# Optimization experiments

Hardware: AMD Instinct MI355X
Metric: run time of the kernel (lower is better)

The kernel has to match this reference:

```python
import jax, jax.numpy as jnp
import numpy as np

N = 131072   # total nodes in batch
D = 128      # hidden dim (in_dim = out_dim = 128)
DX = 64      # raw node feature dim (x and rw_feature each)
NG = 1024    # number of graphs (global_add_pool segments)
E = 4194304  # edges per hop adjacency (avg degree 32)
H = 4        # num_hops + 1 MLP branches per layer


def setup_inputs() -> dict:
    key = jax.random.key(0)
    ks = jax.random.split(key, 16)
    s = 0.05
    return {
        "x": jax.random.normal(ks[0], (N, DX), jnp.float32),
        "rw_feature": jax.random.normal(ks[1], (N, DX), jnp.float32),
        "hop1_features": jax.random.normal(ks[2], (N, D), jnp.float32),
        "hop2_features": jax.random.normal(ks[3], (N, D), jnp.float32),
        "hop3_features": jax.random.normal(ks[4], (N, D), jnp.float32),
        "hop1_edges": jax.random.randint(ks[5], (2, E), 0, N, dtype=jnp.int32),
        "hop2_edges": jax.random.randint(ks[6], (2, E), 0, N, dtype=jnp.int32),
        "hop3_edges": jax.random.randint(ks[7], (2, E), 0, N, dtype=jnp.int32),
        "batch": jnp.sort(jax.random.randint(ks[8], (N,), 0, NG, dtype=jnp.int32)),
        "l1_w1": jax.random.normal(ks[9], (H, D, D), jnp.float32) * s,
        "l1_b1": jnp.zeros((H, D), jnp.float32),
        "l1_w2": jax.random.normal(ks[10], (H, D, D), jnp.float32) * s,
        "l1_b2": jnp.zeros((H, D), jnp.float32),
        "l2_w1": jax.random.normal(ks[11], (H, D, D), jnp.float32) * s,
        "l2_b1": jnp.zeros((H, D), jnp.float32),
        "l2_w2": jax.random.normal(ks[12], (H, D, D), jnp.float32) * s,
        "l2_b2": jnp.zeros((H, D), jnp.float32),
        "lin_w": jax.random.normal(ks[13], (2 * D, D), jnp.float32) * s,
        "lin_b": jnp.zeros((D,), jnp.float32),
    }


def _mhc_layer(hops, w1, b1, w2, b2):
    # hops: [H, N, D]; per-hop MLP (Linear -> ReLU -> Dropout(eval) -> Linear), summed over hops
    z = jax.nn.relu(jnp.einsum('hni,hio->hno', hops, w1) + b1[:, None, :])
    y = jnp.einsum('hno,hop->hnp', z, w2) + b2[:, None, :]
    return jnp.sum(y, axis=0)  # [N, D]


def _spmm(edges, x):
    # torch.sparse.mm(A, x) with A[r, c] = 1.0 per edge; duplicate edges accumulate (COO sum)
    return jax.ops.segment_sum(x[edges[1]], edges[0], num_segments=N)


def reference(x, rw_feature, hop1_features, hop2_features, hop3_features,
              hop1_edges, hop2_edges, hop3_edges, batch,
              l1_w1, l1_b1, l1_w2, l1_b2, l2_w1, l2_b1, l2_w2, l2_b2,
              lin_w, lin_b):
    f = jnp.concatenate([x, rw_feature], axis=1)  # [N, D]
    h1 = jnp.stack([f, hop1_features, hop2_features, hop3_features], axis=0)  # [H, N, D]
    x1 = _mhc_layer(h1, l1_w1, l1_b1, l1_w2, l1_b2)
    h2 = jnp.stack([x1,
                    _spmm(hop1_edges, x1),
                    _spmm(hop2_edges, x1),
                    _spmm(hop3_edges, x1)], axis=0)
    x2 = _mhc_layer(h2, l2_w1, l2_b1, l2_w2, l2_b2)
    out = jnp.concatenate([x1, x2], axis=1) @ lin_w + lin_b  # concat=True path
    return jax.ops.segment_sum(out, batch, num_segments=NG)  # global_add_pool -> [NG, D]
```

## Files before the change

### kernel.cpp

```cpp
#include <hip/hip_runtime.h>

#define N_NODES 131072
#define DIM     128
#define NGRAPH  1024
#define NEDGE   4194304

#define NW      512
#define WBINS   256
#define NSL     256
#define SLICE_E (NEDGE / NSL)
#define CAP     12288

typedef float floatx4 __attribute__((ext_vector_type(4)));
typedef float f32x4  __attribute__((ext_vector_type(4)));
typedef __bf16 bf16x8 __attribute__((ext_vector_type(8)));
typedef __bf16 bf16x4 __attribute__((ext_vector_type(4)));

__device__ __forceinline__ int lds_off(int row, int kb) {
    return row * 256 + (kb ^ ((row & 7) << 4));
}

#define GLOAD16(gp, lp) __builtin_amdgcn_global_load_lds( \
    (const __attribute__((address_space(1))) void*)(gp),  \
    (__attribute__((address_space(3))) void*)(lp), 16, 0, 0)

__device__ __forceinline__ void stage_async(char* dstbase, const char* src,
                                            int w, int lane) {
#pragma unroll
    for (int it = 0; it < 8; ++it) {
        int chunk = it * 4 + w;
        int p = chunk * 1024 + lane * 16;
        int r = p >> 8;
        int o = p & 255;
        const char* g = src + r * 256 + (o ^ ((r & 7) << 4));
        GLOAD16(g, dstbase + chunk * 1024);
    }
}

__global__ __launch_bounds__(256)
void zero_kernel(floatx4* __restrict__ p, long n4) {
    long i = (long)blockIdx.x * blockDim.x + threadIdx.x;
    long stride = (long)gridDim.x * blockDim.x;
    floatx4 z = {0.f, 0.f, 0.f, 0.f};
    for (; i < n4; i += stride) p[i] = z;
}

__global__ __launch_bounds__(256)
void cvt_kernel(const float* __restrict__ src, __bf16* __restrict__ dst) {
    int i = blockIdx.x * 256 + threadIdx.x;
    const int stride = gridDim.x * 256;
    const int total = N_NODES * 32;
    for (; i < total; i += stride) {
        floatx4 v = ((const floatx4*)src)[i];
        bf16x4 h;
        h[0] = (__bf16)v[0]; h[1] = (__bf16)v[1];
        h[2] = (__bf16)v[2]; h[3] = (__bf16)v[3];
        ((bf16x4*)dst)[i] = h;
    }
}

__global__ __launch_bounds__(256)
void cvt_cat_kernel(const float* __restrict__ x, const float* __restrict__ rw,
                    __bf16* __restrict__ dst) {
    int i = blockIdx.x * 256 + threadIdx.x;
    const int stride = gridDim.x * 256;
    const int total = N_NODES * 32;
    for (; i < total; i += stride) {
        int rowg = i >> 5, g = i & 31;
        const float* s = (g < 16) ? x  + (size_t)rowg * 64 + g * 4
                                  : rw + (size_t)rowg * 64 + (g - 16) * 4;
        floatx4 v = *(const floatx4*)s;
        bf16x4 h;
        h[0] = (__bf16)v[0]; h[1] = (__bf16)v[1];
        h[2] = (__bf16)v[2]; h[3] = (__bf16)v[3];
        *(bf16x4*)(dst + (size_t)rowg * 128 + g * 4) = h;
    }
}

__global__ __launch_bounds__(256)
void tr_kernel(const float* __restrict__ src, __bf16* __restrict__ dst, int nmat) {
    int idx = blockIdx.x * blockDim.x + threadIdx.x;
    int total = nmat * 16384;
    if (idx >= total) return;
    int m = idx >> 14;
    int col = (idx >> 7) & 127;
    int k = idx & 127;
    dst[idx] = (__bf16)src[m * 16384 + k * 128 + col];
}

__global__ __launch_bounds__(256)
void wincount_kernel(const int* __restrict__ e1, const int* __restrict__ e2,
                     const int* __restrict__ e3, int* __restrict__ gcount) {
    const int gb = blockIdx.x;
    const int sl = gb % NSL;
    const int hop = gb / NSL;
    const int* rows = hop == 0 ? e1 : hop == 1 ? e2 : e3;

    __shared__ int cnt[NW];
    for (int i = threadIdx.x; i < NW; i += 256) cnt[i] = 0;
    __syncthreads();

    const int4* src = (const int4*)rows + (size_t)sl * (SLICE_E / 4);
    for (int j = threadIdx.x; j < SLICE_E / 4; j += 256) {
        int4 v = src[j];
        atomicAdd(&cnt[v.x >> 8], 1); atomicAdd(&cnt[v.y >> 8], 1);
        atomicAdd(&cnt[v.z >> 8], 1); atomicAdd(&cnt[v.w >> 8], 1);
    }
    __syncthreads();

    int* dst = gcount + ((size_t)hop * NSL + sl) * NW;
    for (int i = threadIdx.x; i < NW; i += 256) dst[i] = cnt[i];
}

__global__ __launch_bounds__(256)
void basescan_kernel(const int* __restrict__ gcount, int* __restrict__ baseo,
                     int* __restrict__ wbase) {
    const int hop = blockIdx.x;
    const int t = threadIdx.x;
    __shared__ int wt[NW];
    __shared__ int part[256];

    for (int k = 0; k < 2; ++k) {
        int w = t * 2 + k;
        int s = 0;
        for (int sl = 0; sl < NSL; ++sl)
            s += gcount[((size_t)hop * NSL + sl) * NW + w];
        wt[w] = s;
    }
    __syncthreads();
    part[t] = wt[2 * t] + wt[2 * t + 1];
    __syncthreads();
    for (int d = 1; d < 256; d <<= 1) {
        int v = (t >= d) ? part[t - d] : 0;
        __syncthreads();
        part[t] += v;
        __syncthreads();
    }
    int run = (t == 0) ? 0 : part[t - 1];
    for (int k = 0; k < 2; ++k) {
        int w = 2 * t + k;
        wbase[hop * (NW + 1) + w] = run;
        int r2 = run;
        for (int sl = 0; sl < NSL; ++sl) {
            baseo[((size_t)hop * NW + w) * NSL + sl] = r2;
            r2 += gcount[((size_t)hop * NSL + sl) * NW + w];
        }
        run += wt[w];
    }
    if (t == 255) wbase[hop * (NW + 1) + NW] = NEDGE;
}

__global__ __launch_bounds__(256)
void bucket_kernel(const int* __restrict__ e1, const int* __restrict__ e2,
                   const int* __restrict__ e3, const int* __restrict__ baseo,
                   int* __restrict__ buf) {
    const int gb = blockIdx.x;
    const int sl = gb % NSL;
    const int hop = gb / NSL;
    const int* rows = hop == 0 ? e1 : hop == 1 ? e2 : e3;
    const int* cs = rows + NEDGE;

    __shared__ int cur[NW];
    for (int i = threadIdx.x; i < NW; i += 256)
        cur[i] = baseo[((size_t)hop * NW + i) * NSL + sl];
    __syncthreads();

    int* b = buf + (size_t)hop * NEDGE;
    const int4* r4 = (const int4*)rows + (size_t)sl * (SLICE_E / 4);
    const int4* c4 = (const int4*)cs + (size_t)sl * (SLICE_E / 4);
    for (int j = threadIdx.x; j < SLICE_E / 4; j += 256) {
        int4 r = r4[j];
        int4 c = c4[j];
        int p;
        p = atomicAdd(&cur[r.x >> 8], 1); b[p] = ((r.x & 255) << 17) | c.x;
        p = atomicAdd(&cur[r.y >> 8], 1); b[p] = ((r.y & 255) << 17) | c.y;
        p = atomicAdd(&cur[r.z >> 8], 1); b[p] = ((r.z & 255) << 17) | c.z;
        p = atomicAdd(&cur[r.w >> 8], 1); b[p] = ((r.w & 255) << 17) | c.w;
    }
}

__global__ __launch_bounds__(256)
void winbuild_kernel(const int* __restrict__ buf, const int* __restrict__ wbase,
                     int* __restrict__ offs3, int* __restrict__ cols) {
    const int gb = blockIdx.x;
    const int w = gb % NW;
    const int hop = gb / NW;
    const int b0 = wbase[hop * (NW + 1) + w];
    const int b1 = wbase[hop * (NW + 1) + w + 1];
    const int tot = b1 - b0;
    const int* src = buf + (size_t)hop * NEDGE + b0;
    int* col = cols + (size_t)hop * NEDGE;
    int* offs = offs3 + (size_t)hop * (N_NODES + 1);
    const int t = threadIdx.x;

    __shared__ int hist[WBINS];
    __shared__ int scanb[WBINS];
    __shared__ int image[CAP];

    hist[t] = 0;
    __syncthreads();
    for (int i = t; i < tot; i += 256) atomicAdd(&hist[src[i] >> 17], 1);
    __syncthreads();

    int v = hist[t];
    scanb[t] = v;
    __syncthreads();
    for (int d = 1; d < 256; d <<= 1) {
        int u = (t >= d) ? scanb[t - d] : 0;
        __syncthreads();
        scanb[t] += u;
        __syncthreads();
    }
    const int excl = scanb[t] - v;

    offs[w * WBINS + t] = b0 + excl;
    if (w == NW - 1 && t == 0) offs[N_NODES] = NEDGE;
    __syncthreads();

    if (tot <= CAP) {
        hist[t] = excl;
        __syncthreads();
        for (int i = t; i < tot; i += 256) {
            int e = src[i];
            int p = atomicAdd(&hist[e >> 17], 1);
            image[p] = e & 0x1FFFF;
        }
        __syncthreads();
        for (int i = t; i < tot; i += 256) col[b0 + i] = image[i];
    } else {
        hist[t] = b0 + excl;
        __syncthreads();
        for (int i = t; i < tot; i += 256) {
            int e = src[i];
            int p = atomicAdd(&hist[e >> 17], 1);
            col[p] = e & 0x1FFFF;
        }
    }
}

__global__ __launch_bounds__(256)
void csr_spmm_kernel(const int* __restrict__ offs, const int* __restrict__ col,
                     const __bf16* __restrict__ xin, __bf16* __restrict__ outb) {
    const int lane = threadIdx.x & 63;
    const int row = blockIdx.x * (blockDim.x >> 6) + (threadIdx.x >> 6);
    if (row >= N_NODES) return;
    const int beg = offs[row];
    const int end = offs[row + 1];

    float a0 = 0.f, a1 = 0.f, b0 = 0.f, b1 = 0.f;
    float c0f = 0.f, c1f = 0.f, d0 = 0.f, d1 = 0.f;
    for (int b = beg; b < end; b += 64) {
        const int n = min(64, end - b);
        int cidx = (b + lane < end) ? col[b + lane] : 0;
        int i = 0;
        for (; i + 4 <= n; i += 4) {
            int e0 = __shfl(cidx, i);
            int e1 = __shfl(cidx, i + 1);
            int e2 = __shfl(cidx, i + 2);
            int e3 = __shfl(cidx, i + 3);
            unsigned v0 = *(const unsigned*)(xin + (size_t)e0 * 128 + lane * 2);
            unsigned v1 = *(const unsigned*)(xin + (size_t)e1 * 128 + lane * 2);
            unsigned v2 = *(const unsigned*)(xin + (size_t)e2 * 128 + lane * 2);
            unsigned v3 = *(const unsigned*)(xin + (size_t)e3 * 128 + lane * 2);
            a0 += __uint_as_float(v0 << 16); a1 += __uint_as_float(v0 & 0xffff0000u);
            b0 += __uint_as_float(v1 << 16); b1 += __uint_as_float(v1 & 0xffff0000u);
            c0f += __uint_as_float(v2 << 16); c1f += __uint_as_float(v2 & 0xffff0000u);
            d0 += __uint_as_float(v3 << 16); d1 += __uint_as_float(v3 & 0xffff0000u);
        }
        for (; i < n; ++i) {
            int e = __shfl(cidx, i);
            unsigned v = *(const unsigned*)(xin + (size_t)e * 128 + lane * 2);
            a0 += __uint_as_float(v << 16); a1 += __uint_as_float(v & 0xffff0000u);
        }
    }
    float o0 = a0 + b0 + c0f + d0;
    float o1 = a1 + b1 + c1f + d1;
    union { unsigned u; __bf16 h[2]; } pk;
    pk.h[0] = (__bf16)o0; pk.h[1] = (__bf16)o1;
    *(unsigned*)(outb + (size_t)row * 128 + lane * 2) = pk.u;
}

__device__ __forceinline__ void mfma_relu_phase(char* az, const char* wb,
                                                const float* bias,
                                                int r0, int lrow, int grp) {
    bf16x8 am[2][4];
#pragma unroll
    for (int mt = 0; mt < 2; ++mt)
#pragma unroll
        for (int kk = 0; kk < 4; ++kk)
            am[mt][kk] = *(const bf16x8*)(az + lds_off(r0 + mt * 16 + lrow,
                                                       kk * 64 + grp * 16));
#pragma unroll
    for (int n = 0; n < 8; ++n) {
        f32x4 a0 = {0.f, 0.f, 0.f, 0.f};
        f32x4 a1 = {0.f, 0.f, 0.f, 0.f};
#pragma unroll
        for (int kk = 0; kk < 4; ++kk) {
            bf16x8 b = *(const bf16x8*)(wb + lds_off(n * 16 + lrow,
                                                     kk * 64 + grp * 16));
            a0 = __builtin_amdgcn_mfma_f32_16x16x32_bf16(am[0][kk], b, a0, 0, 0, 0);
            a1 = __builtin_amdgcn_mfma_f32_16x16x32_bf16(am[1][kk], b, a1, 0, 0, 0);
        }
        float bs = bias[n * 16 + lrow];
#pragma unroll
        for (int rg = 0; rg < 4; ++rg) {
            float v0 = fmaxf(a0[rg] + bs, 0.f);
            float v1 = fmaxf(a1[rg] + bs, 0.f);
            *(__bf16*)(az + lds_off(r0 + grp * 4 + rg, (n * 16 + lrow) * 2)) = (__bf16)v0;
            *(__bf16*)(az + lds_off(r0 + 16 + grp * 4 + rg, (n * 16 + lrow) * 2)) = (__bf16)v1;
        }
    }
}

__device__ __forceinline__ void mfma_phase(const char* az, const char* wb,
                                           int r0, int lrow, int grp,
                                           f32x4 (&acc)[2][8]) {
    bf16x8 am[2][4];
#pragma unroll
    for (int mt = 0; mt < 2; ++mt)
#pragma unroll
        for (int kk = 0; kk < 4; ++kk)
            am[mt][kk] = *(const bf16x8*)(az + lds_off(r0 + mt * 16 + lrow,
                                                       kk * 64 + grp * 16));
#pragma unroll
    for (int kk = 0; kk < 4; ++kk)
#pragma unroll
        for (int n = 0; n < 8; ++n) {
            bf16x8 b = *(const bf16x8*)(wb + lds_off(n * 16 + lrow,
                                                     kk * 64 + grp * 16));
#pragma unroll
            for (int mt = 0; mt < 2; ++mt)
                acc[mt][n] = __builtin_amdgcn_mfma_f32_16x16x32_bf16(
                    am[mt][kk], b, acc[mt][n], 0, 0, 0);
        }
}

__global__ __launch_bounds__(256, 2)
void layer1_kernel(const __bf16* __restrict__ xr, const __bf16* __restrict__ f1,
                   const __bf16* __restrict__ f2, const __bf16* __restrict__ f3,
                   const __bf16* __restrict__ wt1, const float* __restrict__ b1,
                   const __bf16* __restrict__ wt2, const float* __restrict__ b2,
                   __bf16* __restrict__ x1out)
{
    __shared__ uint4 lds_u4[4096];
    char* AZ = (char*)lds_u4;
    char* WB = (char*)lds_u4 + 32768;
    const int tid = threadIdx.x;
    const int lane = tid & 63;
    const int w = tid >> 6;
    const int r0 = w * 32;
    const int lrow = lane & 15;
    const int grp = lane >> 4;
    const int row0 = blockIdx.x * 128;

    f32x4 Y[2][8];
#pragma unroll
    for (int mt = 0; mt < 2; ++mt)
#pragma unroll
        for (int n = 0; n < 8; ++n) Y[mt][n] = {0.f, 0.f, 0.f, 0.f};

    for (int h = 0; h < 4; ++h) {
        const __bf16* feat = (h == 0) ? xr : (h == 1) ? f1 : (h == 2) ? f2 : f3;
        __syncthreads();
        stage_async(AZ, (const char*)(feat + (size_t)row0 * 128), w, lane);
        stage_async(WB, (const char*)(wt1 + (size_t)h * 16384), w, lane);
        __syncthreads();

        mfma_relu_phase(AZ, WB, b1 + h * 128, r0, lrow, grp);

        __syncthreads();
        stage_async(WB, (const char*)(wt2 + (size_t)h * 16384), w, lane);
        __syncthreads();
        mfma_phase(AZ, WB, r0, lrow, grp, Y);
    }

#pragma unroll
    for (int n = 0; n < 8; ++n) {
        int cc = n * 16 + lrow;
        float bs = b2[cc] + b2[128 + cc] + b2[256 + cc] + b2[384 + cc];
#pragma unroll
        for (int mt = 0; mt < 2; ++mt)
#pragma unroll
            for (int rg = 0; rg < 4; ++rg) {
                int zr = r0 + mt * 16 + grp * 4 + rg;
                *(__bf16*)(AZ + lds_off(zr, cc * 2)) = (__bf16)(Y[mt][n][rg] + bs);
            }
    }
    __syncthreads();
#pragma unroll
    for (int it = 0; it < 8; ++it) {
        int f = tid + it * 256;
        int r = f >> 4, o = f & 15;
        uint4 v = *(const uint4*)(AZ + lds_off(r, o * 16));
        *(uint4*)(x1out + (size_t)(row0 + r) * 128 + o * 8) = v;
    }
}

__global__ __launch_bounds__(256, 2)
void layer2_kernel(const __bf16* __restrict__ x1b, const __bf16* __restrict__ s1,
                   const __bf16* __restrict__ s2, const __bf16* __restrict__ s3,
                   const __bf16* __restrict__ wt1, const float* __restrict__ b1,
                   const __bf16* __restrict__ wt2, const float* __restrict__ b2,
                   const __bf16* __restrict__ wtl, const float* __restrict__ linb,
                   const int* __restrict__ batch, float* __restrict__ dout)
{
    __shared__ uint4 lds_u4[4096];
    char* AZ = (char*)lds_u4;
    char* WB = (char*)lds_u4 + 32768;
    const int tid = threadIdx.x;
    const int lane = tid & 63;
    const int w = tid >> 6;
    const int r0 = w * 32;
    const int lrow = lane & 15;
    const int grp = lane >> 4;
    const int row0 = blockIdx.x * 128;

    f32x4 Y[2][8];
#pragma unroll
    for (int mt = 0; mt < 2; ++mt)
#pragma unroll
        for (int n = 0; n < 8; ++n) Y[mt][n] = {0.f, 0.f, 0.f, 0.f};

    for (int h = 0; h < 4; ++h) {
        const __bf16* feat = (h == 0) ? x1b : (h == 1) ? s1 : (h == 2) ? s2 : s3;
        __syncthreads();
        stage_async(AZ, (const char*)(feat + (size_t)row0 * 128), w, lane);
        stage_async(WB, (const char*)(wt1 + (size_t)h * 16384), w, lane);
        __syncthreads();

        mfma_relu_phase(AZ, WB, b1 + h * 128, r0, lrow, grp);

        __syncthreads();
        stage_async(WB, (const char*)(wt2 + (size_t)h * 16384), w, lane);
        __syncthreads();
        mfma_phase(AZ, WB, r0, lrow, grp, Y);
    }

#pragma unroll
    for (int n = 0; n < 8; ++n) {
        int cc = n * 16 + lrow;
        float bs = b2[cc] + b2[128 + cc] + b2[256 + cc] + b2[384 + cc];
#pragma unroll
        for (int mt = 0; mt < 2; ++mt)
#pragma unroll
            for (int rg = 0; rg < 4; ++rg) {
                float v = Y[mt][n][rg] + bs;
                int zr = r0 + mt * 16 + grp * 4 + rg;
                *(__bf16*)(AZ + lds_off(zr, (n * 16 + lrow) * 2)) = (__bf16)v;
            }
    }
    __syncthreads();
    stage_async(WB, (const char*)(wtl + 16384), w, lane);
    __syncthreads();

    f32x4 o[2][8];
#pragma unroll
    for (int mt = 0; mt < 2; ++mt)
#pragma unroll
        for (int n = 0; n < 8; ++n) o[mt][n] = {0.f, 0.f, 0.f, 0.f};
    mfma_phase(AZ, WB, r0, lrow, grp, o);

    __syncthreads();
    stage_async(AZ, (const char*)(x1b + (size_t)row0 * 128), w, lane);
    stage_async(WB, (const char*)wtl, w, lane);
    __syncthreads();
    mfma_phase(AZ, WB, r0, lrow, grp, o);

    __syncthreads();
    float* tile32 = (float*)lds_u4;
#pragma unroll
    for (int n = 0; n < 8; ++n) {
        int cc = n * 16 + lrow;
        float lb = linb[cc];
#pragma unroll
        for (int mt = 0; mt < 2; ++mt)
#pragma unroll
            for (int rg = 0; rg < 4; ++rg) {
                int rl = r0 + mt * 16 + grp * 4 + rg;
                tile32[rl * 128 + cc] = o[mt][n][rg] + lb;
            }
    }
    __syncthreads();

    if (tid < 128) {
        const int d = tid;
        float acc = 0.f;
        int cur = batch[row0];
        for (int r = 0; r < 128; ++r) {
            int b = batch[row0 + r];
            if (b != cur) {
                atomicAdd(dout + (size_t)cur * 128 + d, acc);
                acc = 0.f;
                cur = b;
            }
            acc += tile32[r * 128 + d];
        }
        atomicAdd(dout + (size_t)cur * 128 + d, acc);
    }
}

extern "C" void kernel_launch(void* const* d_in, const int* in_sizes, int n_in,
                              void* d_out, int out_size, void* d_ws, size_t ws_size,
                              hipStream_t stream) {
    (void)in_sizes; (void)n_in; (void)out_size; (void)ws_size;

    const float* x    = (const float*)d_in[0];
    const float* rw   = (const float*)d_in[1];
    const float* f1   = (const float*)d_in[2];
    const float* f2   = (const float*)d_in[3];
    const float* f3   = (const float*)d_in[4];
    const int*   e1   = (const int*)d_in[5];
    const int*   e2   = (const int*)d_in[6];
    const int*   e3   = (const int*)d_in[7];
    const int*   batch= (const int*)d_in[8];
    const float* l1w1 = (const float*)d_in[9];
    const float* l1b1 = (const float*)d_in[10];
    const float* l1w2 = (const float*)d_in[11];
    const float* l1b2 = (const float*)d_in[12];
    const float* l2w1 = (const float*)d_in[13];
    const float* l2b1 = (const float*)d_in[14];
    const float* l2w2 = (const float*)d_in[15];
    const float* l2b2 = (const float*)d_in[16];
    const float* linw = (const float*)d_in[17];
    const float* linb = (const float*)d_in[18];

    float* out = (float*)d_out;

    __bf16* x1b = (__bf16*)d_ws;
    __bf16* s1b = x1b + (size_t)N_NODES * 128;
    __bf16* s2b = s1b + (size_t)N_NODES * 128;
    __bf16* s3b = s2b + (size_t)N_NODES * 128;
    __bf16* wt  = s3b + (size_t)N_NODES * 128;
    __bf16* wt_l1w1 = wt;
    __bf16* wt_l1w2 = wt + 4 * 16384;
    __bf16* wt_l2w1 = wt + 8 * 16384;
    __bf16* wt_l2w2 = wt + 12 * 16384;
    __bf16* wt_lin  = wt + 16 * 16384;
    int* ibase  = (int*)(wt + 18 * 16384);
    int* offs3  = ibase;
    int* gcount = offs3 + (size_t)3 * (N_NODES + 1);
    int* baseo  = gcount + (size_t)3 * NSL * NW;
    int* wbase  = baseo + (size_t)3 * NW * NSL;
    int* buf    = wbase + (size_t)3 * (NW + 1);
    int* cols   = buf + (size_t)3 * NEDGE;
    __bf16* xrb = (__bf16*)buf;

    tr_kernel<<<256, 256, 0, stream>>>(l1w1, wt_l1w1, 4);
    tr_kernel<<<256, 256, 0, stream>>>(l1w2, wt_l1w2, 4);
    tr_kernel<<<256, 256, 0, stream>>>(l2w1, wt_l2w1, 4);
    tr_kernel<<<256, 256, 0, stream>>>(l2w2, wt_l2w2, 4);
    tr_kernel<<<128, 256, 0, stream>>>(linw, wt_lin, 2);

    cvt_cat_kernel<<<4096, 256, 0, stream>>>(x, rw, xrb);
    cvt_kernel<<<4096, 256, 0, stream>>>(f1, s1b);
    cvt_kernel<<<4096, 256, 0, stream>>>(f2, s2b);
    cvt_kernel<<<4096, 256, 0, stream>>>(f3, s3b);

    zero_kernel<<<64, 256, 0, stream>>>((floatx4*)out, (long)NGRAPH * 32);

    layer1_kernel<<<N_NODES / 128, 256, 0, stream>>>(
        xrb, s1b, s2b, s3b, wt_l1w1, l1b1, wt_l1w2, l1b2, x1b);

    wincount_kernel<<<3 * NSL, 256, 0, stream>>>(e1, e2, e3, gcount);
    basescan_kernel<<<3, 256, 0, stream>>>(gcount, baseo, wbase);
    bucket_kernel<<<3 * NSL, 256, 0, stream>>>(e1, e2, e3, baseo, buf);
    winbuild_kernel<<<3 * NW, 256, 0, stream>>>(buf, wbase, offs3, cols);

    __bf16* ss[3] = {s1b, s2b, s3b};
    for (int hop = 0; hop < 3; ++hop) {
        csr_spmm_kernel<<<N_NODES / 4, 256, 0, stream>>>(
            offs3 + (size_t)hop * (N_NODES + 1), cols + (size_t)hop * NEDGE,
            x1b, ss[hop]);
    }

    layer2_kernel<<<N_NODES / 128, 256, 0, stream>>>(
        x1b, s1b, s2b, s3b, wt_l2w1, l2b1, wt_l2w2, l2b2, wt_lin, linb, batch, out);
}
```

Baseline: 958.1 us.

## Stage bucketed edges in LDS before writing contiguous runs to global

The bucket kernel now builds a local histogram and prefix sum per slice, scatters the packed edges into an LDS image sorted by window, and then writes each window's run to global memory in contiguous order. The old scattered per-edge global writes become near-coalesced. The slice count is doubled so each slice's image (8192 ints, 32KB) fits in LDS. The cost is a second read of the row indices, several barriers and a binary search per output element, and more bucket blocks and offset entries.

```diff
diff --git a/kernel.cpp b/kernel.cpp
--- a/kernel.cpp
+++ b/kernel.cpp
@@ -7,7 +7,7 @@
 
 #define NW      512
 #define WBINS   256
-#define NSL     256
+#define NSL     512
 #define SLICE_E (NEDGE / NSL)
 #define CAP     12288
 
@@ -159,23 +159,64 @@
     const int hop = gb / NSL;
     const int* rows = hop == 0 ? e1 : hop == 1 ? e2 : e3;
     const int* cs = rows + NEDGE;
-
-    __shared__ int cur[NW];
-    for (int i = threadIdx.x; i < NW; i += 256)
-        cur[i] = baseo[((size_t)hop * NW + i) * NSL + sl];
-    __syncthreads();
-
-    int* b = buf + (size_t)hop * NEDGE;
+    const int t = threadIdx.x;
+
+    __shared__ int hist[NW];
+    __shared__ int segstart[NW + 1];
+    __shared__ int part[256];
+    __shared__ int image[SLICE_E];
+
+    for (int i = t; i < NW; i += 256) hist[i] = 0;
+    __syncthreads();
+
     const int4* r4 = (const int4*)rows + (size_t)sl * (SLICE_E / 4);
     const int4* c4 = (const int4*)cs + (size_t)sl * (SLICE_E / 4);
-    for (int j = threadIdx.x; j < SLICE_E / 4; j += 256) {
+    for (int j = t; j < SLICE_E / 4; j += 256) {
+        int4 v = r4[j];
+        atomicAdd(&hist[v.x >> 8], 1); atomicAdd(&hist[v.y >> 8], 1);
+        atomicAdd(&hist[v.z >> 8], 1); atomicAdd(&hist[v.w >> 8], 1);
+    }
+    __syncthreads();
+
+    int a = hist[2 * t], b = hist[2 * t + 1];
+    part[t] = a + b;
+    __syncthreads();
+    for (int d = 1; d < 256; d <<= 1) {
+        int v = (t >= d) ? part[t - d] : 0;
+        __syncthreads();
+        part[t] += v;
+        __syncthreads();
+    }
+    int base = (t == 0) ? 0 : part[t - 1];
+    segstart[2 * t] = base;
+    segstart[2 * t + 1] = base + a;
+    if (t == 255) segstart[NW] = SLICE_E;
+    __syncthreads();
+    hist[2 * t] = base;
+    hist[2 * t + 1] = base + a;
+    __syncthreads();
+
+    for (int j = t; j < SLICE_E / 4; j += 256) {
         int4 r = r4[j];
         int4 c = c4[j];
         int p;
-        p = atomicAdd(&cur[r.x >> 8], 1); b[p] = ((r.x & 255) << 17) | c.x;
-        p = atomicAdd(&cur[r.y >> 8], 1); b[p] = ((r.y & 255) << 17) | c.y;
-        p = atomicAdd(&cur[r.z >> 8], 1); b[p] = ((r.z & 255) << 17) | c.z;
-        p = atomicAdd(&cur[r.w >> 8], 1); b[p] = ((r.w & 255) << 17) | c.w;
+        p = atomicAdd(&hist[r.x >> 8], 1); image[p] = ((r.x & 255) << 17) | c.x;
+        p = atomicAdd(&hist[r.y >> 8], 1); image[p] = ((r.y & 255) << 17) | c.y;
+        p = atomicAdd(&hist[r.z >> 8], 1); image[p] = ((r.z & 255) << 17) | c.z;
+        p = atomicAdd(&hist[r.w >> 8], 1); image[p] = ((r.w & 255) << 17) | c.w;
+    }
+    __syncthreads();
+
+    int* bufh = buf + (size_t)hop * NEDGE;
+    const int* bo = baseo + (size_t)hop * NW * NSL + sl;
+    for (int j = t; j < SLICE_E; j += 256) {
+        int lo = 0, hi = NW;
+        while (hi - lo > 1) {
+            int mid = (lo + hi) >> 1;
+            if (segstart[mid] <= j) lo = mid; else hi = mid;
+        }
+        int dst = bo[(size_t)lo * NSL] + (j - segstart[lo]);
+        bufh[dst] = image[j];
     }
 }
 
```

Measured after the change: 908.9 us. -5.1%, faster.
